# Optimization experiments

Measured on AMD Instinct MI355X. Metric: run time of the kernel, lower is better.

## Reference

```python
import jax, jax.numpy as jnp
import numpy as np

MULTI_N_NUM = 2  # hardcoded in FCR.__init__
EPS = 1e-07


def setup_inputs() -> dict:
    key = jax.random.key(0)
    ka, kp, kn, ki = jax.random.split(key, 4)
    B, C, H, W = 32, 3, 256, 256
    a = jax.random.normal(ka, (B, C, H, W), dtype=jnp.float32)
    p = jax.random.normal(kp, (B, C, H, W), dtype=jnp.float32)
    n = jax.random.normal(kn, (B, C, H, W), dtype=jnp.float32)
    # sample_with_j(B, 2, i) -> [i, random j != i]; deterministic materialization
    offs = jax.random.randint(ki, (B, MULTI_N_NUM - 1), 1, B)  # in [1, B-1]
    base = jnp.arange(B, dtype=jnp.int64)
    other = (base[:, None] + offs.astype(jnp.int64)) % B
    neg_idx = jnp.concatenate([base[:, None], other], axis=1)  # [B, 2]
    return {"a": a, "p": p, "n": n, "neg_idx": neg_idx}


def reference(a, p, n, neg_idx):
    # FFT2 over the last two dims -> complex64
    a_fft = jnp.fft.fft2(a)
    p_fft = jnp.fft.fft2(p)
    n_fft = jnp.fft.fft2(n)
    # d_ap[i] = mean |a_fft[i] - p_fft[i]| over (C, H, W)
    d_ap = jnp.mean(jnp.abs(a_fft - p_fft), axis=(1, 2, 3))  # [B]
    # d_an[i, k] = mean |a_fft[i] - n_fft[neg_idx[i, k]]|
    n_gather = n_fft[neg_idx]                                  # [B, K, C, H, W]
    d_an = jnp.mean(jnp.abs(a_fft[:, None] - n_gather), axis=(2, 3, 4))  # [B, K]
    contrastive = jnp.sum(d_ap[:, None] / (d_an + EPS))
    return contrastive / (MULTI_N_NUM * a.shape[0])
```

## Files before the change

### kernel.cpp

```cpp
#include <hip/hip_runtime.h>
#include <hip/hip_fp16.h>
#include <math.h>

#define PIDX(e) ((e) + ((e) >> 4))

#define WAVE_SYNC()                          \
    do {                                     \
        __builtin_amdgcn_wave_barrier();     \
        asm volatile("" ::: "memory");       \
    } while (0)

__device__ __forceinline__ float2 cadd(float2 a, float2 b) { return {a.x + b.x, a.y + b.y}; }
__device__ __forceinline__ float2 csub(float2 a, float2 b) { return {a.x - b.x, a.y - b.y}; }
__device__ __forceinline__ float2 cmul(float2 a, float2 b) {
    return {a.x * b.x - a.y * b.y, a.x * b.y + a.y * b.x};
}

__device__ __forceinline__ void fft256_wave(float2* X, float2* Y, int t) {
    float2* sbuf = X;
    float2* dbuf = Y;
#pragma unroll
    for (int s = 0; s < 4; ++s) {
        const int sh = 2 * s;
        const int mm = 1 << sh;
        const int ll = 64 >> sh;
        const int jj = t >> sh;
        const int kk = t & (mm - 1);
        float2 c0 = sbuf[PIDX(kk + mm * jj)];
        float2 c1 = sbuf[PIDX(kk + mm * (jj + ll))];
        float2 c2 = sbuf[PIDX(kk + mm * (jj + 2 * ll))];
        float2 c3 = sbuf[PIDX(kk + mm * (jj + 3 * ll))];
        float2 sa = cadd(c0, c2);
        float2 sb = csub(c0, c2);
        float2 sc = cadd(c1, c3);
        float2 sd = {c1.y - c3.y, c3.x - c1.x};
        float2 d0 = cadd(sa, sc);
        float2 d1 = cadd(sb, sd);
        float2 d2 = csub(sa, sc);
        float2 d3 = csub(sb, sd);
        const float ang = -0.024543692606170259f * (float)(jj << sh);
        float sy, cx;
        __sincosf(ang, &sy, &cx);
        float2 w1 = {cx, sy};
        float2 w2 = cmul(w1, w1);
        float2 w3 = cmul(w2, w1);
        const int ob = kk + 4 * mm * jj;
        dbuf[PIDX(ob)] = d0;
        dbuf[PIDX(ob + mm)] = cmul(w1, d1);
        dbuf[PIDX(ob + 2 * mm)] = cmul(w2, d2);
        dbuf[PIDX(ob + 3 * mm)] = cmul(w3, d3);
        WAVE_SYNC();
        float2* tmp = sbuf;
        sbuf = dbuf;
        dbuf = tmp;
    }
}

__global__ __launch_bounds__(256) void k_rowfft(const float* __restrict__ A,
                                                const float* __restrict__ P,
                                                const float* __restrict__ N,
                                                const int* __restrict__ negIdx,
                                                __half2* __restrict__ ws, int img0) {
    __shared__ float2 Xb[4][272];
    __shared__ float2 Yb[4][272];
    __shared__ __half2 outT[128 * 33];

    const int img = img0 + blockIdx.y;
    const int pair = img / 3;
    const int ch = img - pair * 3;
    int i, jn;
    const float* S;
    if (pair < 32) {
        i = pair;
        jn = pair;
        S = P;
    } else {
        const int t2 = pair - 32;
        i = t2 >> 1;
        jn = negIdx[(i << 1) + (t2 & 1)];
        S = N;
    }
    const float* abase = A + ((size_t)(i * 3 + ch) << 16);
    const float* sbase = S + ((size_t)(jn * 3 + ch) << 16);

    const int tid = threadIdx.x;
    const int w = tid >> 6;
    const int t = tid & 63;
    const int r0 = blockIdx.x * 32;

    for (int it = 0; it < 4; ++it) {
        const int prl = it * 4 + w;
        const int slot = 2 * prl;
        const int r = r0 + slot;
        const float4 a0 = *(const float4*)(abase + (r << 8) + (t << 2));
        const float4 a1 = *(const float4*)(abase + ((r + 1) << 8) + (t << 2));
        const float4 s0 = *(const float4*)(sbase + (r << 8) + (t << 2));
        const float4 s1 = *(const float4*)(sbase + ((r + 1) << 8) + (t << 2));
        const int e0 = t << 2;
        Xb[w][PIDX(e0 + 0)] = {a0.x - s0.x, a1.x - s1.x};
        Xb[w][PIDX(e0 + 1)] = {a0.y - s0.y, a1.y - s1.y};
        Xb[w][PIDX(e0 + 2)] = {a0.z - s0.z, a1.z - s1.z};
        Xb[w][PIDX(e0 + 3)] = {a0.w - s0.w, a1.w - s1.w};
        WAVE_SYNC();
        fft256_wave(Xb[w], Yb[w], t);
        {
            const float2 p = Xb[w][PIDX(t)];
            if (t == 0) {
                const float2 z128 = Xb[w][PIDX(128)];
                outT[0 * 33 + slot] = __floats2half2_rn(p.x, z128.x);
                outT[0 * 33 + slot + 1] = __floats2half2_rn(p.y, z128.y);
            } else {
                const float2 m = Xb[w][PIDX(256 - t)];
                outT[t * 33 + slot] = __floats2half2_rn(0.5f * (p.x + m.x), 0.5f * (p.y - m.y));
                outT[t * 33 + slot + 1] =
                    __floats2half2_rn(0.5f * (p.y + m.y), -0.5f * (p.x - m.x));
            }
        }
        {
            const int v = t + 64;
            const float2 p = Xb[w][PIDX(v)];
            const float2 m = Xb[w][PIDX(192 - t)];
            outT[v * 33 + slot] = __floats2half2_rn(0.5f * (p.x + m.x), 0.5f * (p.y - m.y));
            outT[v * 33 + slot + 1] = __floats2half2_rn(0.5f * (p.y + m.y), -0.5f * (p.x - m.x));
        }
        WAVE_SYNC();
    }

    __syncthreads();

    __half2* g = ws + (size_t)blockIdx.y * (128 * 256);
    for (int e = tid; e < 128 * 32; e += 256) {
        const int v = e >> 5, rl = e & 31;
        g[v * 256 + r0 + rl] = outT[v * 33 + rl];
    }
}

__global__ __launch_bounds__(256) void k_colfft(const __half2* __restrict__ ws,
                                                float* __restrict__ partial, int img0) {
    __shared__ float2 Xb[4][272];
    __shared__ float2 Yb[4][272];
    __shared__ float wsum[4];
    const int tid = threadIdx.x;
    const int w = tid >> 6, t = tid & 63;
    const int v = blockIdx.x * 4 + w;
    const __half2* g = ws + ((size_t)blockIdx.y * 128 + v) * 256;
    const float4 raw = *(const float4*)(g + 4 * t);
    const __half2* hp = (const __half2*)&raw;
#pragma unroll
    for (int k = 0; k < 4; ++k) {
        const float2 z = __half22float2(hp[k]);
        Xb[w][PIDX(4 * t + k)] = z;
    }
    WAVE_SYNC();
    fft256_wave(Xb[w], Yb[w], t);
    float ssum = 0.f;
    if (v == 0) {
#pragma unroll
        for (int q = 0; q < 4; ++q) {
            const int u = t + 64 * q;
            const float2 zu = Xb[w][PIDX(u)];
            const float2 zm = Xb[w][PIDX((256 - u) & 255)];
            const float ax = 0.5f * (zu.x + zm.x), ay = 0.5f * (zu.y - zm.y);
            const float bx = 0.5f * (zu.y + zm.y), by = -0.5f * (zu.x - zm.x);
            ssum += sqrtf(ax * ax + ay * ay) + sqrtf(bx * bx + by * by);
        }
    } else {
#pragma unroll
        for (int q = 0; q < 4; ++q) {
            const float2 z = Xb[w][PIDX(t + 64 * q)];
            ssum += 2.f * sqrtf(z.x * z.x + z.y * z.y);
        }
    }
#pragma unroll
    for (int off = 32; off; off >>= 1) ssum += __shfl_down(ssum, off);
    if (t == 0) wsum[w] = ssum;
    __syncthreads();
    if (tid == 0) {
        const int img = img0 + blockIdx.y;
        partial[img * 32 + blockIdx.x] = wsum[0] + wsum[1] + wsum[2] + wsum[3];
    }
}

__global__ void k_final(const float* __restrict__ partial, float* __restrict__ out) {
    __shared__ float ps[96];
    const int t = threadIdx.x;
    if (t < 96) {
        float s = 0.f;
        const float* p = partial + t * 96;
        for (int e = 0; e < 96; ++e) s += p[e];
        ps[t] = s;
    }
    __syncthreads();
    if (t < 64) {
        const float inv = 1.f / 196608.f;
        const float dap = ps[t >> 1] * inv;
        const float dan = ps[32 + t] * inv + 1e-7f;
        float val = dap / dan;
#pragma unroll
        for (int off = 32; off; off >>= 1) val += __shfl_down(val, off);
        if (t == 0) out[0] = val * (1.f / 64.f);
    }
}

extern "C" void kernel_launch(void* const* d_in, const int* in_sizes, int n_in,
                              void* d_out, int out_size, void* d_ws, size_t ws_size,
                              hipStream_t stream) {
    const float* A = (const float*)d_in[0];
    const float* P = (const float*)d_in[1];
    const float* N = (const float*)d_in[2];
    const int* negIdx = (const int*)d_in[3];

    float* partial = (float*)d_ws;
    __half2* inter = (__half2*)((char*)d_ws + 40960);
    const size_t perImg = (size_t)128 * 256 * sizeof(__half2);
    size_t avail = ws_size > 40960 ? ws_size - 40960 : 0;
    int cap = (int)(avail / perImg);
    if (cap > 288) cap = 288;
    if (cap < 1) cap = 1;

    for (int img0 = 0; img0 < 288; img0 += cap) {
        const int nimg = (288 - img0 < cap) ? (288 - img0) : cap;
        dim3 g1(8, nimg);
        k_rowfft<<<g1, dim3(256), 0, stream>>>(A, P, N, negIdx, inter, img0);
        dim3 g2(32, nimg);
        k_colfft<<<g2, dim3(256), 0, stream>>>(inter, partial, img0);
    }
    k_final<<<1, 128, 0, stream>>>(partial, (float*)d_out);
}
```

Before: 56.48 us.

## Prefetch next rows in FFT loops, vectorize transpose stores, batch columns per wave

The row FFT kernel now loads the next pair of rows into registers while the current FFT runs, and writes its transposed output with 16-byte stores instead of 4-byte stores. The column FFT kernel now makes each wave handle four columns in a loop with a register prefetch. Its grid shrinks from 32 to 8 blocks per image, and the partial-sum indexing and final reduction are adjusted to match. The intent is to hide global memory latency and reduce store transactions, at the cost of more registers and fewer column blocks, which lowers parallelism.

```diff
diff --git a/kernel.cpp b/kernel.cpp
--- a/kernel.cpp
+++ b/kernel.cpp
@@ -56,6 +56,15 @@
     }
 }
 
+__device__ __forceinline__ void load4(const float* __restrict__ abase,
+                                      const float* __restrict__ sbase, int r, int t, float4& a0,
+                                      float4& a1, float4& s0, float4& s1) {
+    a0 = *(const float4*)(abase + (r << 8) + (t << 2));
+    a1 = *(const float4*)(abase + ((r + 1) << 8) + (t << 2));
+    s0 = *(const float4*)(sbase + (r << 8) + (t << 2));
+    s1 = *(const float4*)(sbase + ((r + 1) << 8) + (t << 2));
+}
+
 __global__ __launch_bounds__(256) void k_rowfft(const float* __restrict__ A,
                                                 const float* __restrict__ P,
                                                 const float* __restrict__ N,
@@ -88,14 +97,13 @@
     const int t = tid & 63;
     const int r0 = blockIdx.x * 32;
 
+    float4 pa0, pa1, ps0, ps1;
+    load4(abase, sbase, r0 + 2 * w, t, pa0, pa1, ps0, ps1);
+
     for (int it = 0; it < 4; ++it) {
-        const int prl = it * 4 + w;
-        const int slot = 2 * prl;
-        const int r = r0 + slot;
-        const float4 a0 = *(const float4*)(abase + (r << 8) + (t << 2));
-        const float4 a1 = *(const float4*)(abase + ((r + 1) << 8) + (t << 2));
-        const float4 s0 = *(const float4*)(sbase + (r << 8) + (t << 2));
-        const float4 s1 = *(const float4*)(sbase + ((r + 1) << 8) + (t << 2));
+        const int slot = 2 * (it * 4 + w);
+        const float4 a0 = pa0, a1 = pa1, s0 = ps0, s1 = ps1;
+        if (it < 3) load4(abase, sbase, r0 + 2 * ((it + 1) * 4 + w), t, pa0, pa1, ps0, ps1);
         const int e0 = t << 2;
         Xb[w][PIDX(e0 + 0)] = {a0.x - s0.x, a1.x - s1.x};
         Xb[w][PIDX(e0 + 1)] = {a0.y - s0.y, a1.y - s1.y};
@@ -129,9 +137,13 @@
     __syncthreads();
 
     __half2* g = ws + (size_t)blockIdx.y * (128 * 256);
-    for (int e = tid; e < 128 * 32; e += 256) {
-        const int v = e >> 5, rl = e & 31;
-        g[v * 256 + r0 + rl] = outT[v * 33 + rl];
+    for (int e = tid; e < 128 * 8; e += 256) {
+        const int v = e >> 3, rl4 = (e & 7) << 2;
+        float4 val;
+        __half2* vp = (__half2*)&val;
+#pragma unroll
+        for (int k = 0; k < 4; ++k) vp[k] = outT[v * 33 + rl4 + k];
+        *(float4*)(g + v * 256 + r0 + rl4) = val;
     }
 }
 
@@ -142,42 +154,51 @@
     __shared__ float wsum[4];
     const int tid = threadIdx.x;
     const int w = tid >> 6, t = tid & 63;
-    const int v = blockIdx.x * 4 + w;
-    const __half2* g = ws + ((size_t)blockIdx.y * 128 + v) * 256;
-    const float4 raw = *(const float4*)(g + 4 * t);
-    const __half2* hp = (const __half2*)&raw;
-#pragma unroll
-    for (int k = 0; k < 4; ++k) {
-        const float2 z = __half22float2(hp[k]);
-        Xb[w][PIDX(4 * t + k)] = z;
-    }
-    WAVE_SYNC();
-    fft256_wave(Xb[w], Yb[w], t);
-    float ssum = 0.f;
-    if (v == 0) {
-#pragma unroll
-        for (int q = 0; q < 4; ++q) {
-            const int u = t + 64 * q;
-            const float2 zu = Xb[w][PIDX(u)];
-            const float2 zm = Xb[w][PIDX((256 - u) & 255)];
-            const float ax = 0.5f * (zu.x + zm.x), ay = 0.5f * (zu.y - zm.y);
-            const float bx = 0.5f * (zu.y + zm.y), by = -0.5f * (zu.x - zm.x);
-            ssum += sqrtf(ax * ax + ay * ay) + sqrtf(bx * bx + by * by);
-        }
-    } else {
-#pragma unroll
-        for (int q = 0; q < 4; ++q) {
-            const float2 z = Xb[w][PIDX(t + 64 * q)];
-            ssum += 2.f * sqrtf(z.x * z.x + z.y * z.y);
-        }
-    }
-#pragma unroll
-    for (int off = 32; off; off >>= 1) ssum += __shfl_down(ssum, off);
-    if (t == 0) wsum[w] = ssum;
+    const int vbase = blockIdx.x * 16 + w * 4;
+    const __half2* gimg = ws + (size_t)blockIdx.y * (128 * 256);
+
+    float acc = 0.f;
+    float4 nraw = *(const float4*)(gimg + (size_t)vbase * 256 + 4 * t);
+    for (int j = 0; j < 4; ++j) {
+        const int v = vbase + j;
+        const float4 raw = nraw;
+        if (j < 3) nraw = *(const float4*)(gimg + (size_t)(v + 1) * 256 + 4 * t);
+        const __half2* hp = (const __half2*)&raw;
+#pragma unroll
+        for (int k = 0; k < 4; ++k) {
+            const float2 z = __half22float2(hp[k]);
+            Xb[w][PIDX(4 * t + k)] = z;
+        }
+        WAVE_SYNC();
+        fft256_wave(Xb[w], Yb[w], t);
+        float ssum = 0.f;
+        if (v == 0) {
+#pragma unroll
+            for (int q = 0; q < 4; ++q) {
+                const int u = t + 64 * q;
+                const float2 zu = Xb[w][PIDX(u)];
+                const float2 zm = Xb[w][PIDX((256 - u) & 255)];
+                const float ax = 0.5f * (zu.x + zm.x), ay = 0.5f * (zu.y - zm.y);
+                const float bx = 0.5f * (zu.y + zm.y), by = -0.5f * (zu.x - zm.x);
+                ssum += sqrtf(ax * ax + ay * ay) + sqrtf(bx * bx + by * by);
+            }
+        } else {
+#pragma unroll
+            for (int q = 0; q < 4; ++q) {
+                const float2 z = Xb[w][PIDX(t + 64 * q)];
+                ssum += 2.f * sqrtf(z.x * z.x + z.y * z.y);
+            }
+        }
+        acc += ssum;
+        WAVE_SYNC();
+    }
+#pragma unroll
+    for (int off = 32; off; off >>= 1) acc += __shfl_down(acc, off);
+    if (t == 0) wsum[w] = acc;
     __syncthreads();
     if (tid == 0) {
         const int img = img0 + blockIdx.y;
-        partial[img * 32 + blockIdx.x] = wsum[0] + wsum[1] + wsum[2] + wsum[3];
+        partial[img * 8 + blockIdx.x] = wsum[0] + wsum[1] + wsum[2] + wsum[3];
     }
 }
 
@@ -186,8 +207,8 @@
     const int t = threadIdx.x;
     if (t < 96) {
         float s = 0.f;
-        const float* p = partial + t * 96;
-        for (int e = 0; e < 96; ++e) s += p[e];
+        const float* p = partial + t * 24;
+        for (int e = 0; e < 24; ++e) s += p[e];
         ps[t] = s;
     }
     __syncthreads();
@@ -222,7 +243,7 @@
         const int nimg = (288 - img0 < cap) ? (288 - img0) : cap;
         dim3 g1(8, nimg);
         k_rowfft<<<g1, dim3(256), 0, stream>>>(A, P, N, negIdx, inter, img0);
-        dim3 g2(32, nimg);
+        dim3 g2(8, nimg);
         k_colfft<<<g2, dim3(256), 0, stream>>>(inter, partial, img0);
     }
     k_final<<<1, 128, 0, stream>>>(partial, (float*)d_out);
```

Result: faster. 50.76 us (-10.1%).
